# Performance work log

Hardware: AMD Instinct MI355X
Metric: run time of the kernel (lower is better)

Reference implementation:

```python
import jax, jax.numpy as jnp
import numpy as np

N_HEADS = 16
HEAD_DIM = 64
ROPE_BASE = 10000.0
EPS = 1e-6


def _rope_tables(T, hd, dtype):
    inv_freq = 1.0 / (ROPE_BASE ** (jnp.arange(0, hd, 2, dtype=jnp.float32) / hd))
    freqs = jnp.arange(T, dtype=jnp.float32)[:, None] * inv_freq[None, :]  # [T, hd/2]
    cos = jnp.cos(freqs)[None, :, None, :].astype(dtype)  # [1,T,1,hd/2]
    sin = jnp.sin(freqs)[None, :, None, :].astype(dtype)
    return cos, sin


def _apply_rope(x, cos, sin):
    d = x.shape[-1] // 2
    x1, x2 = x[..., :d], x[..., d:]
    return jnp.concatenate([x1 * cos + x2 * sin, -x1 * sin + x2 * cos], axis=-1)


def setup_inputs() -> dict:
    key = jax.random.key(0)
    k1, k2, k3, k4 = jax.random.split(key, 4)
    B, T, C = 4, 1024, 1024
    x = jax.random.normal(k1, (B, T, C), dtype=jnp.float32)
    W_qkv = jax.random.normal(k2, (3 * C, C), dtype=jnp.float32) * (1.0 / np.sqrt(C))
    W_out = jax.random.normal(k3, (C, C), dtype=jnp.float32) * (1.0 / np.sqrt(C))
    # learnable per-head curvature, init = exp(randn) * base_curvature (base=1.0)
    hyp_k = jnp.exp(jax.random.normal(k4, (1, N_HEADS, 1, 1), dtype=jnp.float32))
    return {"x": x, "W_qkv": W_qkv, "W_out": W_out, "hyp_k": hyp_k}


def reference(x, W_qkv, W_out, hyp_k):
    B, T, C = x.shape
    H, hd = N_HEADS, HEAD_DIM
    qkv = x @ W_qkv.T  # [B,T,3C]
    q, k, v = jnp.split(qkv, 3, axis=-1)
    q = q.reshape(B, T, H, hd)
    k = k.reshape(B, T, H, hd)
    v = v.reshape(B, T, H, hd)

    cos, sin = _rope_tables(T, hd, x.dtype)
    q = _apply_rope(q, cos, sin)
    k = _apply_rope(k, cos, sin)

    # [B,H,T,hd]
    q = q.transpose(0, 2, 1, 3)
    k = k.transpose(0, 2, 1, 3)
    v = v.transpose(0, 2, 1, 3)

    # Lorentz lift: x0 = sqrt(k + ||x||^2); inner = -x0*y0 + <x,y>;
    # dist = sqrt(k) * arccosh(-inner / k)  (geoopt Lorentz convention)
    kc = hyp_k[:, :, :, 0]  # [1,H,1]
    q0 = jnp.sqrt(kc + jnp.sum(q * q, axis=-1))  # [B,H,T]
    k0 = jnp.sqrt(kc + jnp.sum(k * k, axis=-1))  # [B,H,T]
    inner = jnp.einsum('bhld,bhsd->bhls', q, k) - q0[..., None] * k0[:, :, None, :]
    arg = jnp.maximum(-inner / hyp_k, 1.0 + EPS)
    dis = jnp.sqrt(hyp_k) * jnp.arccosh(arg)  # [B,H,L,S]

    attn_weight = 1.0 / (EPS + dis)
    causal = jnp.tril(jnp.ones((T, T), dtype=bool))
    attn_weight = jnp.where(causal, attn_weight, -jnp.inf)
    attn = jax.nn.softmax(attn_weight, axis=-1)
    out = jnp.einsum('bhls,bhsd->bhld', attn, v)  # [B,H,T,hd]
    out = out.transpose(0, 2, 1, 3).reshape(B, T, C)
    return out @ W_out.T
```

## Files before the change

### kernel.cpp

```cpp
#include <hip/hip_runtime.h>

#define B_ 4
#define T_ 1024
#define C_ 1024
#define H_ 16
#define HD_ 64

typedef short bf16x8 __attribute__((ext_vector_type(8)));
typedef float f32x4 __attribute__((ext_vector_type(4)));

__device__ __forceinline__ ushort f2bf(float f) {
    union { float f; unsigned u; } v; v.f = f;
    unsigned u = v.u;
    unsigned r = (u + 0x7fffu + ((u >> 16) & 1u)) >> 16;
    return (ushort)r;
}

__device__ __forceinline__ f32x4 mfma16(bf16x8 a, bf16x8 b, f32x4 c) {
    return __builtin_amdgcn_mfma_f32_16x16x32_bf16(a, b, c, 0, 0, 0);
}

__device__ __forceinline__ bf16x8 lds_frag(const ushort* base, int row, int byteoff) {
    int addr = (row * 128 + byteoff) ^ ((row & 7) << 4);
    uint4 u = *(const uint4*)((const char*)base + addr);
    return __builtin_bit_cast(bf16x8, u);
}

__device__ __forceinline__ bf16x8 lds_frag_v(const ushort* base, int d, int byteoff) {
    int addr = (d * 128 + byteoff) ^ ((((d & 7) ^ (d >> 3)) & 7) << 4);
    uint4 u = *(const uint4*)((const char*)base + addr);
    return __builtin_bit_cast(bf16x8, u);
}

__device__ __forceinline__ bf16x8 lds_frag_p(const ushort* base, int row, int byteoff) {
    int addr = (row * 128 + byteoff) ^ (((row >> 2) & 3) << 5);
    uint4 u = *(const uint4*)((const char*)base + addr);
    return __builtin_bit_cast(bf16x8, u);
}

__device__ __forceinline__ void bar_lds() {
    asm volatile("s_waitcnt lgkmcnt(0)" ::: "memory");
    __builtin_amdgcn_sched_barrier(0);
    __builtin_amdgcn_s_barrier();
    __builtin_amdgcn_sched_barrier(0);
}

__global__ void cast_all(const float* __restrict__ x, const float* __restrict__ wqkv,
                         const float* __restrict__ wout,
                         ushort* __restrict__ xb, ushort* __restrict__ wqkvb,
                         ushort* __restrict__ woutb) {
    int i = (blockIdx.x * 256 + threadIdx.x) * 4;
    const float* src; ushort* dst; int off;
    if (i < 4194304)      { src = x;    dst = xb;    off = i; }
    else if (i < 7340032) { src = wqkv; dst = wqkvb; off = i - 4194304; }
    else                  { src = wout; dst = woutb; off = i - 7340032; }
    float4 v = *(const float4*)(src + off);
    ushort4 o = make_ushort4(f2bf(v.x), f2bf(v.y), f2bf(v.z), f2bf(v.w));
    *(ushort4*)(dst + off) = o;
}

#define GEMM_COMPUTE_128x64(As, Bs)                                                       \
    {                                                                                     \
        _Pragma("unroll")                                                                 \
        for (int ks = 0; ks < 2; ++ks) {                                                  \
            bf16x8 af[2], bfr[4];                                                         \
            _Pragma("unroll")                                                             \
            for (int mf = 0; mf < 2; ++mf)                                                \
                af[mf] = lds_frag(As, wv * 32 + mf * 16 + (lane & 15),                    \
                                  ks * 64 + ((lane >> 4) << 4));                          \
            _Pragma("unroll")                                                             \
            for (int nf = 0; nf < 4; ++nf)                                                \
                bfr[nf] = lds_frag(Bs, nf * 16 + (lane & 15),                             \
                                   ks * 64 + ((lane >> 4) << 4));                         \
            _Pragma("unroll")                                                             \
            for (int mf = 0; mf < 2; ++mf)                                                \
                _Pragma("unroll")                                                         \
                for (int nf = 0; nf < 4; ++nf)                                            \
                    acc[mf][nf] = mfma16(af[mf], bfr[nf], acc[mf][nf]);                   \
        }                                                                                 \
    }

#define GEMM_DBUF_STAGING(Asrc, Bsrc)                                                     \
    const int srow = tid >> 3, soff = (tid & 7) * 8;                                      \
    const int swz = (srow & 7) << 4;                                                      \
    uint4 a0, a1, a2, a3, b0, b1;                                                         \
    auto issue = [&](int kt) {                                                            \
        const ushort* Ap = Asrc + kt * 64;                                                \
        const ushort* Bp = Bsrc + kt * 64;                                                \
        a0 = *(const uint4*)(Ap + (size_t)srow * C_ + soff);                              \
        a1 = *(const uint4*)(Ap + (size_t)(32 + srow) * C_ + soff);                       \
        a2 = *(const uint4*)(Ap + (size_t)(64 + srow) * C_ + soff);                       \
        a3 = *(const uint4*)(Ap + (size_t)(96 + srow) * C_ + soff);                       \
        b0 = *(const uint4*)(Bp + (size_t)srow * C_ + soff);                              \
        b1 = *(const uint4*)(Bp + (size_t)(32 + srow) * C_ + soff);                       \
    };                                                                                    \
    auto lwrite = [&](ushort* Ad, ushort* Bd) {                                           \
        *(uint4*)((char*)Ad + ((tid * 16) ^ swz)) = a0;                                   \
        *(uint4*)((char*)Ad + (((tid + 256) * 16) ^ swz)) = a1;                           \
        *(uint4*)((char*)Ad + (((tid + 512) * 16) ^ swz)) = a2;                           \
        *(uint4*)((char*)Ad + (((tid + 768) * 16) ^ swz)) = a3;                           \
        *(uint4*)((char*)Bd + ((tid * 16) ^ swz)) = b0;                                   \
        *(uint4*)((char*)Bd + (((tid + 256) * 16) ^ swz)) = b1;                           \
    }

#define GEMM_DBUF_LOOP()                                                                  \
    issue(0);                                                                             \
    lwrite(As0, Bs0);                                                                     \
    issue(1);                                                                             \
    bar_lds();                                                                            \
    for (int kt = 0; kt < 12; kt += 2) {                                                  \
        lwrite(As1, Bs1);                                                                 \
        issue(kt + 2);                                                                    \
        GEMM_COMPUTE_128x64(As0, Bs0);                                                    \
        bar_lds();                                                                        \
        lwrite(As0, Bs0);                                                                 \
        issue(kt + 3);                                                                    \
        GEMM_COMPUTE_128x64(As1, Bs1);                                                    \
        bar_lds();                                                                        \
    }                                                                                     \
    lwrite(As1, Bs1);                                                        \
    issue(14);                                                                            \
    GEMM_COMPUTE_128x64(As0, Bs0);                                           \
    bar_lds();                                                                            \
    lwrite(As0, Bs0);                                                        \
    issue(15);                                                                            \
    GEMM_COMPUTE_128x64(As1, Bs1);                                           \
    bar_lds();                                                                            \
    lwrite(As1, Bs1);                                                        \
    GEMM_COMPUTE_128x64(As0, Bs0);                                           \
    bar_lds();                                                                            \
    GEMM_COMPUTE_128x64(As1, Bs1);

__global__ __launch_bounds__(256) void gemm_qkv(
    const ushort* __restrict__ Xb, const ushort* __restrict__ Wb,
    const float* __restrict__ hyp,
    ushort* __restrict__ Qo, ushort* __restrict__ Ko, ushort* __restrict__ Vo,
    float* __restrict__ q0g, float* __restrict__ k0g)
{
    __shared__ ushort As0[128 * 64], Bs0[64 * 64];
    __shared__ ushort As1[128 * 64], Bs1[64 * 64];
    const int tid = threadIdx.x, lane = tid & 63, wv = tid >> 6;
    const int m0 = blockIdx.x * 128, n0 = blockIdx.y * 64;
    const ushort* Asrc = Xb + (size_t)m0 * C_;
    const ushort* Bsrc = Wb + (size_t)n0 * C_;

    GEMM_DBUF_STAGING(Asrc, Bsrc);

    f32x4 acc[2][4] = {};
    GEMM_DBUF_LOOP();

    const int sector = n0 >> 10;
    const int h = (n0 & 1023) >> 6;
    const float kc = hyp[h];
    const float inv_k = 1.0f / kc;
    float invf[2];
    invf[0] = __expf(-0.28782313662425572f * (float)(lane & 15));
    invf[1] = __expf(-0.28782313662425572f * (float)(16 + (lane & 15)));

#pragma unroll
    for (int mf = 0; mf < 2; ++mf) {
        float o[4][4];
#pragma unroll
        for (int nf = 0; nf < 4; ++nf)
#pragma unroll
            for (int r = 0; r < 4; ++r) o[nf][r] = acc[mf][nf][r];

        if (sector < 2) {
#pragma unroll
            for (int p = 0; p < 2; ++p) {
#pragma unroll
                for (int r = 0; r < 4; ++r) {
                    int m = m0 + wv * 32 + mf * 16 + ((lane >> 4) << 2) + r;
                    int t = m & (T_ - 1);
                    float sn, cs; __sincosf((float)t * invf[p], &sn, &cs);
                    float x1 = o[p][r], x2 = o[p + 2][r];
                    o[p][r]     =  x1 * cs + x2 * sn;
                    o[p + 2][r] = -x1 * sn + x2 * cs;
                }
            }
        }

#pragma unroll
        for (int r = 0; r < 4; ++r) {
            int m = m0 + wv * 32 + mf * 16 + ((lane >> 4) << 2) + r;
            int b = m >> 10, t = m & (T_ - 1);
            int bh = b * H_ + h;
            size_t base = ((size_t)bh * T_ + t) * HD_;
            float nrm = 0.f;
#pragma unroll
            for (int nf = 0; nf < 4; ++nf) {
                int d = nf * 16 + (lane & 15);
                float v = o[nf][r];
                nrm += v * v;
                ushort bv = f2bf(sector == 1 ? v * inv_k : v);
                if (sector == 0)      Qo[base + d] = bv;
                else if (sector == 1) Ko[base + d] = bv;
                else                  Vo[base + d] = bv;
            }
            if (sector < 2) {
#pragma unroll
                for (int mk = 1; mk < 16; mk <<= 1) nrm += __shfl_xor(nrm, mk);
                if ((lane & 15) == 0) {
                    float v0 = sqrtf(kc + nrm);
                    if (sector == 0) q0g[(size_t)bh * T_ + t] = v0;
                    else             k0g[(size_t)bh * T_ + t] = v0 * inv_k;
                }
            }
        }
    }
}

__global__ __launch_bounds__(256, 2) void attn_fwd(
    const ushort* __restrict__ Q, const ushort* __restrict__ K, const ushort* __restrict__ V,
    const float* __restrict__ q0g, const float* __restrict__ k0g,
    const float* __restrict__ hyp, ushort* __restrict__ AO)
{
    __shared__ ushort Ks[64 * 64];
    __shared__ ushort Vts[64 * 64];
    __shared__ ushort Ps[4][16 * 64];
    __shared__ float k0s[64];

    const int tid = threadIdx.x, lane = tid & 63, wv = tid >> 6;
    const int pr = blockIdx.x >> 6;
    const int bh = blockIdx.x & 63;
    const int h = bh & (H_ - 1);
    const int qa = pr, qb = 15 - pr, nt = qb + 1;
    const float c3 = sqrtf(hyp[h]) * 0.48045301391820142f;
    const float e3 = 6.931471805599453e-07f;

    const ushort* Kb = K + (size_t)bh * T_ * HD_;
    const ushort* Vb = V + (size_t)bh * T_ * HD_;

    bf16x8 aqA[2], aqB[2];
    {
        const ushort* qA = Q + ((size_t)bh * T_ + qa * 64 + wv * 16 + (lane & 15)) * HD_;
        const ushort* qB = Q + ((size_t)bh * T_ + qb * 64 + wv * 16 + (lane & 15)) * HD_;
#pragma unroll
        for (int ks = 0; ks < 2; ++ks) {
            aqA[ks] = __builtin_bit_cast(bf16x8, *(const uint4*)(qA + ks * 32 + ((lane >> 4) << 3)));
            aqB[ks] = __builtin_bit_cast(bf16x8, *(const uint4*)(qB + ks * 32 + ((lane >> 4) << 3)));
        }
    }
    float q0A[4], q0B[4];
#pragma unroll
    for (int r = 0; r < 4; ++r) {
        int rr = wv * 16 + ((lane >> 4) << 2) + r;
        q0A[r] = q0g[(size_t)bh * T_ + qa * 64 + rr];
        q0B[r] = q0g[(size_t)bh * T_ + qb * 64 + rr];
    }

    f32x4 oaccA[4] = {}, oaccB[4] = {};
    float lpA[4] = {}, lpB[4] = {};

    const int krow = tid >> 3, koff = tid & 7;
    const int sp = tid >> 3, dc = tid & 7;
    uint4 kv0, kv1, vv0, vv1;
    float kz = 0.f;
    auto issue = [&](int s0) {
        kv0 = *(const uint4*)(Kb + (size_t)(s0 + krow) * HD_ + koff * 8);
        kv1 = *(const uint4*)(Kb + (size_t)(s0 + 32 + krow) * HD_ + koff * 8);
        vv0 = *(const uint4*)(Vb + (size_t)(s0 + 2 * sp) * HD_ + dc * 8);
        vv1 = *(const uint4*)(Vb + (size_t)(s0 + 2 * sp + 1) * HD_ + dc * 8);
        if (tid < 64) kz = k0g[(size_t)bh * T_ + s0 + tid];
    };

    auto geom = [&](const f32x4* sc, const float* q0, const float* k0r, float p[4][4]) {
#pragma unroll
        for (int r = 0; r < 4; ++r)
#pragma unroll
            for (int sf = 0; sf < 4; ++sf) {
                float arg = fmaf(q0[r], k0r[sf], -sc[sf][r]);
                arg = fmaxf(arg, 1.0f + 1e-6f);
                float t = fmaf(arg, arg, -1.0f);
                float u = arg + __builtin_amdgcn_sqrtf(t);
                float l2 = __builtin_amdgcn_logf(u);
                float w2 = fmaf(l2, c3, e3);
                float rv = fminf(__builtin_amdgcn_rcpf(w2), 30.0f);
                p[sf][r] = __builtin_amdgcn_exp2f(rv);
            }
    };
    auto mask_diag = [&](float p[4][4]) {
        const int qloc = wv * 16 + ((lane >> 4) << 2);
#pragma unroll
        for (int r = 0; r < 4; ++r)
#pragma unroll
            for (int sf = 0; sf < 4; ++sf)
                if (sf * 16 + (lane & 15) > qloc + r) p[sf][r] = 0.f;
    };
    auto pv_step = [&](float p[4][4], ushort* ps, const bf16x8 (&vf)[2][4],
                       f32x4* oacc, float* lp) {
#pragma unroll
        for (int r = 0; r < 4; ++r) {
            int row = ((lane >> 4) << 2) + r;
#pragma unroll
            for (int sf = 0; sf < 4; ++sf) {
                int addr = (row * 128 + (sf * 16 + (lane & 15)) * 2) ^ (((row >> 2) & 3) << 5);
                *(ushort*)((char*)ps + addr) = f2bf(p[sf][r]);
            }
            lp[r] += (p[0][r] + p[1][r]) + (p[2][r] + p[3][r]);
        }
#pragma unroll
        for (int ks = 0; ks < 2; ++ks) {
            bf16x8 ap = lds_frag_p(ps, lane & 15, ks * 64 + ((lane >> 4) << 4));
#pragma unroll
            for (int df = 0; df < 4; ++df)
                oacc[df] = mfma16(ap, vf[ks][df], oacc[df]);
        }
    };

    issue(0);

    for (int it = 0; it < nt; ++it) {
        const bool actA = (it <= qa);
        __syncthreads();
        {
            *(uint4*)((char*)Ks + ((tid * 16) ^ ((krow & 7) << 4))) = kv0;
            int c1 = tid + 256;
            *(uint4*)((char*)Ks + ((c1 * 16) ^ (((c1 >> 3) & 7) << 4))) = kv1;
            union { uint4 v; ushort u[8]; } a, b;
            a.v = vv0; b.v = vv1;
#pragma unroll
            for (int j = 0; j < 8; ++j) {
                int d = dc * 8 + j;
                uint pack = (uint)a.u[j] | ((uint)b.u[j] << 16);
                *(uint*)((char*)Vts + ((d * 128 + sp * 4) ^ (((j ^ dc) & 7) << 4))) = pack;
            }
            if (tid < 64) k0s[tid] = kz;
        }
        if (it + 1 < nt) issue((it + 1) * 64);
        __syncthreads();

        bf16x8 bk[2][4];
#pragma unroll
        for (int ks = 0; ks < 2; ++ks)
#pragma unroll
            for (int sf = 0; sf < 4; ++sf)
                bk[ks][sf] = lds_frag(Ks, sf * 16 + (lane & 15), ks * 64 + ((lane >> 4) << 4));

        float k0r[4];
#pragma unroll
        for (int sf = 0; sf < 4; ++sf) k0r[sf] = k0s[sf * 16 + (lane & 15)];

        f32x4 scB[4] = {};
#pragma unroll
        for (int ks = 0; ks < 2; ++ks)
#pragma unroll
            for (int sf = 0; sf < 4; ++sf)
                scB[sf] = mfma16(aqB[ks], bk[ks][sf], scB[sf]);
        f32x4 scA[4] = {};
        if (actA) {
#pragma unroll
            for (int ks = 0; ks < 2; ++ks)
#pragma unroll
                for (int sf = 0; sf < 4; ++sf)
                    scA[sf] = mfma16(aqA[ks], bk[ks][sf], scA[sf]);
        }

        bf16x8 vf[2][4];
#pragma unroll
        for (int ks = 0; ks < 2; ++ks)
#pragma unroll
            for (int df = 0; df < 4; ++df)
                vf[ks][df] = lds_frag_v(Vts, df * 16 + (lane & 15), ks * 64 + ((lane >> 4) << 4));

        float pB[4][4];
        geom(scB, q0B, k0r, pB);
        if (it == qb) mask_diag(pB);
        pv_step(pB, Ps[wv], vf, oaccB, lpB);

        if (actA) {
            float pA[4][4];
            geom(scA, q0A, k0r, pA);
            if (it == qa) mask_diag(pA);
            pv_step(pA, Ps[wv], vf, oaccA, lpA);
        }
    }

    const int b = bh >> 4;
    auto epi = [&](f32x4* oacc, float* lp, int qt) {
#pragma unroll
        for (int r = 0; r < 4; ++r) {
            float s = lp[r];
#pragma unroll
            for (int mk = 1; mk < 16; mk <<= 1) s += __shfl_xor(s, mk);
            float invl = __builtin_amdgcn_rcpf(s);
            int t = qt * 64 + wv * 16 + ((lane >> 4) << 2) + r;
            size_t base = ((size_t)b * T_ + t) * C_ + h * HD_;
#pragma unroll
            for (int df = 0; df < 4; ++df)
                AO[base + df * 16 + (lane & 15)] = f2bf(oacc[df][r] * invl);
        }
    };
    epi(oaccA, lpA, qa);
    epi(oaccB, lpB, qb);
}

__global__ __launch_bounds__(256) void gemm_out(
    const ushort* __restrict__ Ab, const ushort* __restrict__ Wb, float* __restrict__ Out)
{
    __shared__ ushort As0[128 * 64], Bs0[64 * 64];
    __shared__ ushort As1[128 * 64], Bs1[64 * 64];
    const int tid = threadIdx.x, lane = tid & 63, wv = tid >> 6;
    const int m0 = blockIdx.x * 128, n0 = blockIdx.y * 64;
    const ushort* Asrc = Ab + (size_t)m0 * C_;
    const ushort* Bsrc = Wb + (size_t)n0 * C_;

    GEMM_DBUF_STAGING(Asrc, Bsrc);

    f32x4 acc[2][4] = {};
    GEMM_DBUF_LOOP();

#pragma unroll
    for (int mf = 0; mf < 2; ++mf)
#pragma unroll
        for (int r = 0; r < 4; ++r) {
            int m = m0 + wv * 32 + mf * 16 + ((lane >> 4) << 2) + r;
#pragma unroll
            for (int nf = 0; nf < 4; ++nf) {
                int n = n0 + nf * 16 + (lane & 15);
                Out[(size_t)m * C_ + n] = acc[mf][nf][r];
            }
        }
}

extern "C" void kernel_launch(void* const* d_in, const int* in_sizes, int n_in,
                              void* d_out, int out_size, void* d_ws, size_t ws_size,
                              hipStream_t stream)
{
    const float* x    = (const float*)d_in[0];
    const float* wqkv = (const float*)d_in[1];
    const float* wout = (const float*)d_in[2];
    const float* hyp  = (const float*)d_in[3];

    char* ws = (char*)d_ws;
    ushort* xb    = (ushort*)(ws + 0);
    ushort* wqkvb = (ushort*)(ws + 8388608);
    ushort* woutb = (ushort*)(ws + 14680064);
    ushort* Qb    = (ushort*)(ws + 16777216);
    ushort* Kb    = (ushort*)(ws + 25165824);
    ushort* Vb    = (ushort*)(ws + 33554432);
    ushort* Ab    = (ushort*)(ws + 41943040);
    float*  q0    = (float*)(ws + 50331648);
    float*  k0    = (float*)(ws + 50593792);

    cast_all<<<8192, 256, 0, stream>>>(x, wqkv, wout, xb, wqkvb, woutb);

    gemm_qkv<<<dim3(32, 48), 256, 0, stream>>>(xb, wqkvb, hyp, Qb, Kb, Vb, q0, k0);
    attn_fwd<<<512, 256, 0, stream>>>(Qb, Kb, Vb, q0, k0, hyp, Ab);
    gemm_out<<<dim3(32, 16), 256, 0, stream>>>(Ab, woutb, (float*)d_out);
}
```

Before: 95.50 us.

## Stage GEMM tiles with direct global-to-LDS loads instead of register staging

Both the QKV and output projection GEMMs now load A and B tiles with global_load_lds, writing straight into shared memory. The global chunk index is XOR-swizzled so the existing fragment reads stay valid. The double-buffered loop is rebuilt around vmcnt waits plus barriers, which removes the VGPR round trip and the separate LDS store instructions. The trade-off is correctness that depends on vmcnt accounting (six loads per stage) and on explicit barriers before a buffer is overwritten; gemm_out is also moved earlier in the file.

```diff
diff --git a/kernel.cpp b/kernel.cpp
--- a/kernel.cpp
+++ b/kernel.cpp
@@ -38,11 +38,47 @@
     return __builtin_bit_cast(bf16x8, u);
 }
 
-__device__ __forceinline__ void bar_lds() {
-    asm volatile("s_waitcnt lgkmcnt(0)" ::: "memory");
+__device__ __forceinline__ void bar_plain() {
     __builtin_amdgcn_sched_barrier(0);
     __builtin_amdgcn_s_barrier();
     __builtin_amdgcn_sched_barrier(0);
+}
+__device__ __forceinline__ void bar_vm6() {
+    asm volatile("s_waitcnt vmcnt(6)" ::: "memory");
+    __builtin_amdgcn_sched_barrier(0);
+    __builtin_amdgcn_s_barrier();
+    __builtin_amdgcn_sched_barrier(0);
+}
+__device__ __forceinline__ void bar_vm0() {
+    asm volatile("s_waitcnt vmcnt(0)" ::: "memory");
+    __builtin_amdgcn_sched_barrier(0);
+    __builtin_amdgcn_s_barrier();
+    __builtin_amdgcn_sched_barrier(0);
+}
+
+__device__ __forceinline__ void stage128(ushort* sbase, const ushort* gtile, int wv, int lane) {
+    const int srow = lane >> 3;
+    const ushort* g0 = gtile + (size_t)srow * C_ + ((((lane & 7) ^ srow)) << 3);
+#pragma unroll
+    for (int i = 0; i < 4; ++i) {
+        int w = wv * 4 + i;
+        const ushort* g = g0 + (size_t)(w * 8) * C_;
+        ushort* l = sbase + w * 512;
+        __builtin_amdgcn_global_load_lds((const __attribute__((address_space(1))) void*)g,
+                                         (__attribute__((address_space(3))) void*)l, 16, 0, 0);
+    }
+}
+__device__ __forceinline__ void stage64(ushort* sbase, const ushort* gtile, int wv, int lane) {
+    const int srow = lane >> 3;
+    const ushort* g0 = gtile + (size_t)srow * C_ + ((((lane & 7) ^ srow)) << 3);
+#pragma unroll
+    for (int i = 0; i < 2; ++i) {
+        int w = wv * 2 + i;
+        const ushort* g = g0 + (size_t)(w * 8) * C_;
+        ushort* l = sbase + w * 512;
+        __builtin_amdgcn_global_load_lds((const __attribute__((address_space(1))) void*)g,
+                                         (__attribute__((address_space(3))) void*)l, 16, 0, 0);
+    }
 }
 
 __global__ void cast_all(const float* __restrict__ x, const float* __restrict__ wqkv,
@@ -80,55 +116,22 @@
         }                                                                                 \
     }
 
-#define GEMM_DBUF_STAGING(Asrc, Bsrc)                                                     \
-    const int srow = tid >> 3, soff = (tid & 7) * 8;                                      \
-    const int swz = (srow & 7) << 4;                                                      \
-    uint4 a0, a1, a2, a3, b0, b1;                                                         \
-    auto issue = [&](int kt) {                                                            \
-        const ushort* Ap = Asrc + kt * 64;                                                \
-        const ushort* Bp = Bsrc + kt * 64;                                                \
-        a0 = *(const uint4*)(Ap + (size_t)srow * C_ + soff);                              \
-        a1 = *(const uint4*)(Ap + (size_t)(32 + srow) * C_ + soff);                       \
-        a2 = *(const uint4*)(Ap + (size_t)(64 + srow) * C_ + soff);                       \
-        a3 = *(const uint4*)(Ap + (size_t)(96 + srow) * C_ + soff);                       \
-        b0 = *(const uint4*)(Bp + (size_t)srow * C_ + soff);                              \
-        b1 = *(const uint4*)(Bp + (size_t)(32 + srow) * C_ + soff);                       \
-    };                                                                                    \
-    auto lwrite = [&](ushort* Ad, ushort* Bd) {                                           \
-        *(uint4*)((char*)Ad + ((tid * 16) ^ swz)) = a0;                                   \
-        *(uint4*)((char*)Ad + (((tid + 256) * 16) ^ swz)) = a1;                           \
-        *(uint4*)((char*)Ad + (((tid + 512) * 16) ^ swz)) = a2;                           \
-        *(uint4*)((char*)Ad + (((tid + 768) * 16) ^ swz)) = a3;                           \
-        *(uint4*)((char*)Bd + ((tid * 16) ^ swz)) = b0;                                   \
-        *(uint4*)((char*)Bd + (((tid + 256) * 16) ^ swz)) = b1;                           \
-    }
-
-#define GEMM_DBUF_LOOP()                                                                  \
-    issue(0);                                                                             \
-    lwrite(As0, Bs0);                                                                     \
-    issue(1);                                                                             \
-    bar_lds();                                                                            \
-    for (int kt = 0; kt < 12; kt += 2) {                                                  \
-        lwrite(As1, Bs1);                                                                 \
-        issue(kt + 2);                                                                    \
+#define GEMM_DMA_LOOP()                                                                   \
+    stage(As0, Bs0, 0);                                                                   \
+    stage(As1, Bs1, 1);                                                                   \
+    for (int kt = 0; kt < 14; kt += 2) {                                                  \
+        bar_vm6();                                     \
         GEMM_COMPUTE_128x64(As0, Bs0);                                                    \
-        bar_lds();                                                                        \
-        lwrite(As0, Bs0);                                                                 \
-        issue(kt + 3);                                                                    \
+        bar_plain();                                     \
+        stage(As0, Bs0, kt + 2);                                                          \
+        bar_vm6();                                                     \
         GEMM_COMPUTE_128x64(As1, Bs1);                                                    \
-        bar_lds();                                                                        \
+        bar_plain();                                                                      \
+        stage(As1, Bs1, kt + 3);                                          \
     }                                                                                     \
-    lwrite(As1, Bs1);                                                        \
-    issue(14);                                                                            \
-    GEMM_COMPUTE_128x64(As0, Bs0);                                           \
-    bar_lds();                                                                            \
-    lwrite(As0, Bs0);                                                        \
-    issue(15);                                                                            \
-    GEMM_COMPUTE_128x64(As1, Bs1);                                           \
-    bar_lds();                                                                            \
-    lwrite(As1, Bs1);                                                        \
-    GEMM_COMPUTE_128x64(As0, Bs0);                                           \
-    bar_lds();                                                                            \
+    bar_vm6();                                            \
+    GEMM_COMPUTE_128x64(As0, Bs0);                                                        \
+    bar_vm0();                                                            \
     GEMM_COMPUTE_128x64(As1, Bs1);
 
 __global__ __launch_bounds__(256) void gemm_qkv(
@@ -144,10 +147,13 @@
     const ushort* Asrc = Xb + (size_t)m0 * C_;
     const ushort* Bsrc = Wb + (size_t)n0 * C_;
 
-    GEMM_DBUF_STAGING(Asrc, Bsrc);
+    auto stage = [&](ushort* Ad, ushort* Bd, int kt) {
+        stage128(Ad, Asrc + kt * 64, wv, lane);
+        stage64(Bd, Bsrc + kt * 64, wv, lane);
+    };
 
     f32x4 acc[2][4] = {};
-    GEMM_DBUF_LOOP();
+    GEMM_DMA_LOOP();
 
     const int sector = n0 >> 10;
     const int h = (n0 & 1023) >> 6;
@@ -208,6 +214,37 @@
             }
         }
     }
+}
+
+__global__ __launch_bounds__(256) void gemm_out(
+    const ushort* __restrict__ Ab, const ushort* __restrict__ Wb, float* __restrict__ Out)
+{
+    __shared__ ushort As0[128 * 64], Bs0[64 * 64];
+    __shared__ ushort As1[128 * 64], Bs1[64 * 64];
+    const int tid = threadIdx.x, lane = tid & 63, wv = tid >> 6;
+    const int m0 = blockIdx.x * 128, n0 = blockIdx.y * 64;
+    const ushort* Asrc = Ab + (size_t)m0 * C_;
+    const ushort* Bsrc = Wb + (size_t)n0 * C_;
+
+    auto stage = [&](ushort* Ad, ushort* Bd, int kt) {
+        stage128(Ad, Asrc + kt * 64, wv, lane);
+        stage64(Bd, Bsrc + kt * 64, wv, lane);
+    };
+
+    f32x4 acc[2][4] = {};
+    GEMM_DMA_LOOP();
+
+#pragma unroll
+    for (int mf = 0; mf < 2; ++mf)
+#pragma unroll
+        for (int r = 0; r < 4; ++r) {
+            int m = m0 + wv * 32 + mf * 16 + ((lane >> 4) << 2) + r;
+#pragma unroll
+            for (int nf = 0; nf < 4; ++nf) {
+                int n = n0 + nf * 16 + (lane & 15);
+                Out[(size_t)m * C_ + n] = acc[mf][nf][r];
+            }
+        }
 }
 
 __global__ __launch_bounds__(256, 2) void attn_fwd(
@@ -395,34 +432,6 @@
     epi(oaccB, lpB, qb);
 }
 
-__global__ __launch_bounds__(256) void gemm_out(
-    const ushort* __restrict__ Ab, const ushort* __restrict__ Wb, float* __restrict__ Out)
-{
-    __shared__ ushort As0[128 * 64], Bs0[64 * 64];
-    __shared__ ushort As1[128 * 64], Bs1[64 * 64];
-    const int tid = threadIdx.x, lane = tid & 63, wv = tid >> 6;
-    const int m0 = blockIdx.x * 128, n0 = blockIdx.y * 64;
-    const ushort* Asrc = Ab + (size_t)m0 * C_;
-    const ushort* Bsrc = Wb + (size_t)n0 * C_;
-
-    GEMM_DBUF_STAGING(Asrc, Bsrc);
-
-    f32x4 acc[2][4] = {};
-    GEMM_DBUF_LOOP();
-
-#pragma unroll
-    for (int mf = 0; mf < 2; ++mf)
-#pragma unroll
-        for (int r = 0; r < 4; ++r) {
-            int m = m0 + wv * 32 + mf * 16 + ((lane >> 4) << 2) + r;
-#pragma unroll
-            for (int nf = 0; nf < 4; ++nf) {
-                int n = n0 + nf * 16 + (lane & 15);
-                Out[(size_t)m * C_ + n] = acc[mf][nf][r];
-            }
-        }
-}
-
 extern "C" void kernel_launch(void* const* d_in, const int* in_sizes, int n_in,
                               void* d_out, int out_size, void* d_ws, size_t ws_size,
                               hipStream_t stream)
```

Result: no change. 93.85 us (-1.7%).
